# Kernel tuning notes

Measured on AMD Instinct MI355X. Metric: run time of the kernel, lower is better.

The kernel has to match this reference:

```python
import math
import jax, jax.numpy as jnp
import numpy as np

POS_RATIO = 0.2
NEG_RATIO = 0.2
LOSS_WEIGHT = 1.0
EPS = 1e-8  # torch.cosine_similarity eps


def setup_inputs() -> dict:
    key = jax.random.key(0)
    x = jax.random.normal(key, (4096, 512), dtype=jnp.float32)
    return {"x": x}


def reference(x) -> jnp.ndarray:
    # Cosine similarity via L2-normalize + GEMM (same math as torch.cosine_similarity
    # with per-row norm clamped at eps), instead of the O(N^2 * D) broadcast form.
    norms = jnp.maximum(jnp.linalg.norm(x, axis=-1, keepdims=True), EPS)
    xn = x / norms                      # [N, D]
    sim = xn @ xn.T                     # [N, N]

    # Thresholds from the sorted (detached) flattened similarity matrix.
    sim_sorted = jnp.sort(jax.lax.stop_gradient(sim).ravel())
    n_total = sim_sorted.shape[0]       # N*N (static)
    pos_thresh = sim_sorted[math.ceil(n_total * (1.0 - POS_RATIO))]
    neg_thresh = sim_sorted[math.ceil(n_total * NEG_RATIO)]

    pos_mask = sim > pos_thresh
    neg_mask = sim < neg_thresh

    # masked means, matching (1 - sim[pos_mask]).clamp_min(0).mean() etc.
    pos_cnt = jnp.sum(pos_mask)
    neg_cnt = jnp.sum(neg_mask)
    pos_loss = jnp.sum(jnp.where(pos_mask, jnp.maximum(1.0 - sim, 0.0), 0.0)) / pos_cnt
    neg_loss = jnp.sum(jnp.where(neg_mask, jnp.maximum(sim, 0.0), 0.0)) / neg_cnt

    return LOSS_WEIGHT * (pos_loss + neg_loss)
```

## Files before the change

### kernel.cpp

```cpp
#include <hip/hip_runtime.h>
#include <hip/hip_bf16.h>
#include <math.h>


#define N 4096
#define D 512
#define NN 16777216u
#define NBF 2048
#define NSLICE 528

typedef __attribute__((ext_vector_type(8))) short bf16x8;
typedef __attribute__((ext_vector_type(4))) float f32x4;
typedef const __attribute__((address_space(1))) void gas_t;
typedef __attribute__((address_space(3))) void las_t;

__device__ __forceinline__ int val2bin(float s) {
  int b = (int)fmaf(s, 1024.0f, 1024.0f);
  return b < 0 ? 0 : (b > NBF - 1 ? NBF - 1 : b);
}
__device__ __forceinline__ unsigned short f2bf(float f) {
  unsigned int u = __float_as_uint(f);
  u += 0x7FFFu + ((u >> 16) & 1u);
  return (unsigned short)(u >> 16);
}

__global__ __launch_bounds__(256) void norm_conv(const float* __restrict__ x,
                                                 unsigned short* __restrict__ xnb) {
  const int row = blockIdx.x;
  const int tid = threadIdx.x;
  const float2 v = ((const float2*)(x + (size_t)row * D))[tid];
  float s = v.x * v.x + v.y * v.y;
#pragma unroll
  for (int o = 32; o > 0; o >>= 1) s += __shfl_xor(s, o);
  __shared__ float wsum[4];
  __shared__ float s_rinv;
  if ((tid & 63) == 0) wsum[tid >> 6] = s;
  __syncthreads();
  if (tid == 0) {
    float t = wsum[0] + wsum[1] + wsum[2] + wsum[3];
    s_rinv = 1.0f / fmaxf(sqrtf(t), 1e-8f);
  }
  __syncthreads();
  const float r = s_rinv;
  ((ushort2*)(xnb + (size_t)row * D))[tid] = make_ushort2(f2bf(v.x * r), f2bf(v.y * r));
}

#define BM 128
#define BK 64
__global__ __launch_bounds__(256, 3) void gemm_fused(const unsigned short* __restrict__ xnb,
                                                     unsigned int* __restrict__ slice_cnt,
                                                     float* __restrict__ slice_top) {
  const int bid = blockIdx.x;
  int by = (int)((sqrtf(8.0f * (float)bid + 1.0f) - 1.0f) * 0.5f);
  while ((by + 1) * (by + 2) / 2 <= bid) ++by;
  while (by * (by + 1) / 2 > bid) --by;
  const int bx = bid - by * (by + 1) / 2;

  __shared__ unsigned short As[BM][BK];
  __shared__ unsigned short Bs[BM][BK];
  __shared__ unsigned int cnt[2][NBF];
  __shared__ float stop;
  const int tid = threadIdx.x;
  for (int i = tid; i < 2 * NBF; i += 256) ((unsigned int*)cnt)[i] = 0u;
  if (tid == 0) stop = 0.f;

  const int w = tid >> 6, l = tid & 63;
  const int wr = w >> 1, wc = w & 1;
  const int lr = l & 15, kgrp = l >> 4;
  const int swz = lr & 7;
  const int hc = w >> 1;
  const int bm = bx * BM, bn = by * BM;

  const int srow = l >> 3;
  const int gsrc = (l & 7) ^ srow;
  const unsigned short* srcA0 = xnb + (size_t)(bm + w * 32 + srow) * D + gsrc * 8;
  const unsigned short* srcB0 = xnb + (size_t)(bn + w * 32 + srow) * D + gsrc * 8;

  f32x4 acc[4][4] = {};

  for (int kt = 0; kt < D; kt += BK) {
    __syncthreads();
#pragma unroll
    for (int c = 0; c < 4; ++c) {
      __builtin_amdgcn_global_load_lds((gas_t*)(srcA0 + (size_t)c * 8 * D + kt),
                                       (las_t*)&As[w * 32 + c * 8][0], 16, 0, 0);
      __builtin_amdgcn_global_load_lds((gas_t*)(srcB0 + (size_t)c * 8 * D + kt),
                                       (las_t*)&Bs[w * 32 + c * 8][0], 16, 0, 0);
    }
    __syncthreads();
#pragma unroll
    for (int kk = 0; kk < BK; kk += 32) {
      const int g0 = (kk >> 3) + kgrp;
      bf16x8 af[4], bf4[4];
#pragma unroll
      for (int m = 0; m < 4; ++m)
        af[m] = *(const bf16x8*)&As[wr * 64 + m * 16 + lr][(g0 ^ swz) * 8];
#pragma unroll
      for (int n = 0; n < 4; ++n)
        bf4[n] = *(const bf16x8*)&Bs[wc * 64 + n * 16 + lr][(g0 ^ swz) * 8];
#pragma unroll
      for (int m = 0; m < 4; ++m)
#pragma unroll
        for (int n = 0; n < 4; ++n)
          acc[m][n] = __builtin_amdgcn_mfma_f32_16x16x32_bf16(af[m], bf4[n], acc[m][n], 0, 0, 0);
    }
  }

  const unsigned int wg = (bx == by) ? 1u : 2u;
  __syncthreads();
#pragma unroll
  for (int m = 0; m < 4; ++m)
#pragma unroll
    for (int n = 0; n < 4; ++n)
#pragma unroll
      for (int e = 0; e < 4; ++e) {
        const float s = acc[m][n][e];
        const int b = val2bin(s);
        atomicAdd(&cnt[hc][b], wg);
        if (b == NBF - 1) atomicAdd(&stop, (float)wg * fmaxf(1.0f - s, 0.0f));
      }
  __syncthreads();
  unsigned int* oc = slice_cnt + (size_t)bid * NBF;
  for (int i = tid; i < NBF; i += 256) oc[i] = cnt[0][i] + cnt[1][i];
  if (tid == 0) slice_top[bid] = stop;
}

__global__ __launch_bounds__(256) void reduce_bins(const unsigned int* __restrict__ slice_cnt,
                                                   unsigned int* __restrict__ cnt_part) {
  const int t = blockIdx.x * 256 + threadIdx.x;
  const int b = t & (NBF - 1);
  const int c = t >> 11;
  const int s0 = c * (NSLICE / 4);
  unsigned int cs = 0;
#pragma unroll 4
  for (int s = 0; s < NSLICE / 4; ++s)
    cs += slice_cnt[(size_t)(s0 + s) * NBF + b];
  cnt_part[t] = cs;
}

__global__ __launch_bounds__(256) void final_loss(const unsigned int* __restrict__ cnt_part,
                                                  const float* __restrict__ slice_top,
                                                  float* __restrict__ out,
                                                  unsigned int kneg, unsigned int kpos) {
  __shared__ unsigned int part[256], Q[256];
  __shared__ unsigned int sbp, sbn;
  __shared__ double tstage[4];
  __shared__ double dstage[2][4];
  __shared__ unsigned int ustage[2][4];
  const int tid = threadIdx.x;
  const int lane = tid & 63, wid = tid >> 6;

  unsigned int c8[8];
  unsigned int tot = 0;
#pragma unroll
  for (int j = 0; j < 8; ++j) {
    const int b = tid * 8 + j;
    unsigned int cc = 0;
#pragma unroll
    for (int c = 0; c < 4; ++c) cc += cnt_part[c * NBF + b];
    c8[j] = cc; tot += cc;
  }
  {
    float tl = 0.f;
    for (int s = tid; s < NSLICE; s += 256) tl += slice_top[s];
    double td = tl;
#pragma unroll
    for (int o = 32; o > 0; o >>= 1) td += __shfl_xor(td, o);
    if (lane == 0) tstage[wid] = td;
  }
  part[tid] = tot;
  Q[tid] = tot;
  __syncthreads();
#pragma unroll
  for (int off = 1; off < 256; off <<= 1) {
    unsigned int t2 = (tid >= off) ? Q[tid - off] : 0u;
    __syncthreads();
    Q[tid] += t2;
    __syncthreads();
  }
  const unsigned int total = Q[255];
  const unsigned int incl = Q[tid];
  const unsigned int excl = incl - part[tid];
  const unsigned int targets[2] = {kpos, kneg};
#pragma unroll
  for (int t = 0; t < 2; ++t) {
    const unsigned int r = (total == 0u) ? 0u
                         : (targets[t] < total ? targets[t] : total - 1u);
    if (total != 0u && excl <= r && r < incl) {
      unsigned int rr = r - excl, cum = 0;
      int bsel = -1;
#pragma unroll
      for (int j = 0; j < 8; ++j) {
        if (bsel < 0 && cum + c8[j] > rr) bsel = j;
        else if (bsel < 0) cum += c8[j];
      }
      if (bsel < 0) bsel = 7;
      if (t == 0) sbp = tid * 8 + (unsigned int)bsel;
      else        sbn = tid * 8 + (unsigned int)bsel;
    }
  }
  __syncthreads();
  const double topsum = tstage[0] + tstage[1] + tstage[2] + tstage[3];
  const unsigned int bp = sbp, bn = sbn;

  double psum = 0.0, nsum = 0.0;
  unsigned int pcnt = 0, ncnt = 0;
#pragma unroll
  for (int j = 0; j < 8; ++j) {
    const unsigned int b = tid * 8 + j;
    const double mid = ((double)b + 0.5) / 1024.0 - 1.0;
    if (b > bp) {
      pcnt += c8[j];
      psum += (b == NBF - 1) ? topsum : (double)c8[j] * (1.0 - mid);
    }
    if (b < bn) {
      ncnt += c8[j];
      if (mid > 0.0) nsum += (double)c8[j] * mid;
    }
  }
#pragma unroll
  for (int o = 32; o > 0; o >>= 1) {
    psum += __shfl_xor(psum, o);
    nsum += __shfl_xor(nsum, o);
    pcnt += __shfl_xor(pcnt, o);
    ncnt += __shfl_xor(ncnt, o);
  }
  if (lane == 0) {
    dstage[0][wid] = psum; dstage[1][wid] = nsum;
    ustage[0][wid] = pcnt; ustage[1][wid] = ncnt;
  }
  __syncthreads();
  if (tid == 0) {
    const double ps = dstage[0][0] + dstage[0][1] + dstage[0][2] + dstage[0][3];
    const double ns = dstage[1][0] + dstage[1][1] + dstage[1][2] + dstage[1][3];
    const unsigned int pc = ustage[0][0] + ustage[0][1] + ustage[0][2] + ustage[0][3];
    const unsigned int nc = ustage[1][0] + ustage[1][1] + ustage[1][2] + ustage[1][3];
    const double pl = pc ? ps / (double)pc : 0.0;
    const double nl = nc ? ns / (double)nc : 0.0;
    out[0] = (float)(pl + nl);
  }
}

extern "C" void kernel_launch(void* const* d_in, const int* in_sizes, int n_in,
                              void* d_out, int out_size, void* d_ws, size_t ws_size,
                              hipStream_t stream) {
  const float* x = (const float*)d_in[0];
  float* out = (float*)d_out;
  char* ws = (char*)d_ws;

  unsigned short* xnb = (unsigned short*)ws;
  size_t off = (size_t)N * D * 2;
  unsigned int* slice_cnt = (unsigned int*)(ws + off);
  off += (size_t)NSLICE * NBF * 4;
  float* slice_top = (float*)(ws + off);
  off += (size_t)NSLICE * 4;
  off = (off + 255) & ~(size_t)255;
  unsigned int* cnt_part = (unsigned int*)(ws + off);

  const unsigned int kneg = (unsigned int)ceil((double)NN * 0.2);
  const unsigned int kpos = (unsigned int)ceil((double)NN * (1.0 - 0.2));

  norm_conv<<<N, 256, 0, stream>>>(x, xnb);
  gemm_fused<<<NSLICE, 256, 0, stream>>>(xnb, slice_cnt, slice_top);
  reduce_bins<<<32, 256, 0, stream>>>(slice_cnt, cnt_part);
  final_loss<<<1, 256, 0, stream>>>(cnt_part, slice_top, out, kneg, kpos);
}
```

Before: 45.22 us.

## Merge histogram slices with global atomics and use one wave per row in normalize

Each GEMM block now atomically adds its nonzero shared-memory bin counts into a single global histogram. This replaces writing 528 per-block slices and removes the separate reduce_bins kernel. The normalization kernel now assigns one wavefront per row with float4 loads and a 16-byte bf16 store, which drops the shared-memory reduction and barriers. The costs are an extra memset launch to zero the histogram and possible atomic contention on global bins.

```diff
diff --git a/kernel.cpp b/kernel.cpp
--- a/kernel.cpp
+++ b/kernel.cpp
@@ -26,29 +26,28 @@
 
 __global__ __launch_bounds__(256) void norm_conv(const float* __restrict__ x,
                                                  unsigned short* __restrict__ xnb) {
-  const int row = blockIdx.x;
-  const int tid = threadIdx.x;
-  const float2 v = ((const float2*)(x + (size_t)row * D))[tid];
-  float s = v.x * v.x + v.y * v.y;
+  const int row = blockIdx.x * 4 + (threadIdx.x >> 6);
+  const int l = threadIdx.x & 63;
+  const float4* rp = (const float4*)(x + (size_t)row * D);
+  const float4 v0 = rp[l * 2];
+  const float4 v1 = rp[l * 2 + 1];
+  float s = v0.x * v0.x + v0.y * v0.y + v0.z * v0.z + v0.w * v0.w +
+            v1.x * v1.x + v1.y * v1.y + v1.z * v1.z + v1.w * v1.w;
 #pragma unroll
   for (int o = 32; o > 0; o >>= 1) s += __shfl_xor(s, o);
-  __shared__ float wsum[4];
-  __shared__ float s_rinv;
-  if ((tid & 63) == 0) wsum[tid >> 6] = s;
-  __syncthreads();
-  if (tid == 0) {
-    float t = wsum[0] + wsum[1] + wsum[2] + wsum[3];
-    s_rinv = 1.0f / fmaxf(sqrtf(t), 1e-8f);
-  }
-  __syncthreads();
-  const float r = s_rinv;
-  ((ushort2*)(xnb + (size_t)row * D))[tid] = make_ushort2(f2bf(v.x * r), f2bf(v.y * r));
+  const float r = 1.0f / fmaxf(sqrtf(s), 1e-8f);
+  bf16x8 o8;
+  o8[0] = (short)f2bf(v0.x * r); o8[1] = (short)f2bf(v0.y * r);
+  o8[2] = (short)f2bf(v0.z * r); o8[3] = (short)f2bf(v0.w * r);
+  o8[4] = (short)f2bf(v1.x * r); o8[5] = (short)f2bf(v1.y * r);
+  o8[6] = (short)f2bf(v1.z * r); o8[7] = (short)f2bf(v1.w * r);
+  *(bf16x8*)&xnb[(size_t)row * D + l * 8] = o8;
 }
 
 #define BM 128
 #define BK 64
 __global__ __launch_bounds__(256, 3) void gemm_fused(const unsigned short* __restrict__ xnb,
-                                                     unsigned int* __restrict__ slice_cnt,
+                                                     unsigned int* __restrict__ hist,
                                                      float* __restrict__ slice_top) {
   const int bid = blockIdx.x;
   int by = (int)((sqrtf(8.0f * (float)bid + 1.0f) - 1.0f) * 0.5f);
@@ -120,25 +119,14 @@
         if (b == NBF - 1) atomicAdd(&stop, (float)wg * fmaxf(1.0f - s, 0.0f));
       }
   __syncthreads();
-  unsigned int* oc = slice_cnt + (size_t)bid * NBF;
-  for (int i = tid; i < NBF; i += 256) oc[i] = cnt[0][i] + cnt[1][i];
+  for (int i = tid; i < NBF; i += 256) {
+    const unsigned int c = cnt[0][i] + cnt[1][i];
+    if (c) atomicAdd(&hist[i], c);
+  }
   if (tid == 0) slice_top[bid] = stop;
 }
 
-__global__ __launch_bounds__(256) void reduce_bins(const unsigned int* __restrict__ slice_cnt,
-                                                   unsigned int* __restrict__ cnt_part) {
-  const int t = blockIdx.x * 256 + threadIdx.x;
-  const int b = t & (NBF - 1);
-  const int c = t >> 11;
-  const int s0 = c * (NSLICE / 4);
-  unsigned int cs = 0;
-#pragma unroll 4
-  for (int s = 0; s < NSLICE / 4; ++s)
-    cs += slice_cnt[(size_t)(s0 + s) * NBF + b];
-  cnt_part[t] = cs;
-}
-
-__global__ __launch_bounds__(256) void final_loss(const unsigned int* __restrict__ cnt_part,
+__global__ __launch_bounds__(256) void final_loss(const unsigned int* __restrict__ hist,
                                                   const float* __restrict__ slice_top,
                                                   float* __restrict__ out,
                                                   unsigned int kneg, unsigned int kpos) {
@@ -154,11 +142,8 @@
   unsigned int tot = 0;
 #pragma unroll
   for (int j = 0; j < 8; ++j) {
-    const int b = tid * 8 + j;
-    unsigned int cc = 0;
-#pragma unroll
-    for (int c = 0; c < 4; ++c) cc += cnt_part[c * NBF + b];
-    c8[j] = cc; tot += cc;
+    c8[j] = hist[tid * 8 + j];
+    tot += c8[j];
   }
   {
     float tl = 0.f;
@@ -250,18 +235,15 @@
 
   unsigned short* xnb = (unsigned short*)ws;
   size_t off = (size_t)N * D * 2;
-  unsigned int* slice_cnt = (unsigned int*)(ws + off);
-  off += (size_t)NSLICE * NBF * 4;
+  unsigned int* hist = (unsigned int*)(ws + off);
+  off += (size_t)NBF * 4;
   float* slice_top = (float*)(ws + off);
-  off += (size_t)NSLICE * 4;
-  off = (off + 255) & ~(size_t)255;
-  unsigned int* cnt_part = (unsigned int*)(ws + off);
 
   const unsigned int kneg = (unsigned int)ceil((double)NN * 0.2);
   const unsigned int kpos = (unsigned int)ceil((double)NN * (1.0 - 0.2));
 
-  norm_conv<<<N, 256, 0, stream>>>(x, xnb);
-  gemm_fused<<<NSLICE, 256, 0, stream>>>(xnb, slice_cnt, slice_top);
-  reduce_bins<<<32, 256, 0, stream>>>(slice_cnt, cnt_part);
-  final_loss<<<1, 256, 0, stream>>>(cnt_part, slice_top, out, kneg, kpos);
-}
+  hipMemsetAsync(hist, 0, (size_t)NBF * 4, stream);
+  norm_conv<<<N / 4, 256, 0, stream>>>(x, xnb);
+  gemm_fused<<<NSLICE, 256, 0, stream>>>(xnb, hist, slice_top);
+  final_loss<<<1, 256, 0, stream>>>(hist, slice_top, out, kneg, kpos);
+}
```

Result: faster. 42.19 us (-6.7%).
